# Performance work log

Measured on AMD Instinct MI355X. Metric: run time of the kernel, lower is better.

Reference implementation:

```python
import jax, jax.numpy as jnp
import numpy as np

HEADS = 8
OUT_C = 8
NEG_SLOPE = 0.2  # PyG GATConv default


def setup_inputs() -> dict:
    key = jax.random.key(0)
    k = jax.random.split(key, 6)
    N, F, E = 100000, 128, 1600000
    x = jax.random.normal(k[0], (N, F), dtype=jnp.float32)
    edge_index = jax.random.randint(k[1], (2, E), 0, N, dtype=jnp.int64)
    W = jax.random.normal(k[2], (F, HEADS * OUT_C), dtype=jnp.float32) * (1.0 / np.sqrt(F))
    att_src = jax.random.normal(k[3], (HEADS, OUT_C), dtype=jnp.float32) * 0.1
    att_dst = jax.random.normal(k[4], (HEADS, OUT_C), dtype=jnp.float32) * 0.1
    bias = jnp.zeros((HEADS * OUT_C,), dtype=jnp.float32)
    return {"x": x, "edge_index": edge_index, "W": W,
            "att_src": att_src, "att_dst": att_dst, "bias": bias}


def reference(x, edge_index, W, att_src, att_dst, bias):
    N = x.shape[0]
    # add self loops (PyG default add_self_loops=True)
    loops = jnp.arange(N, dtype=edge_index.dtype)
    src = jnp.concatenate([edge_index[0], loops])  # [E']
    dst = jnp.concatenate([edge_index[1], loops])  # [E']

    h = (x @ W).reshape(N, HEADS, OUT_C)          # [N,H,C]
    a_src = jnp.einsum('nhc,hc->nh', h, att_src)  # [N,H]
    a_dst = jnp.einsum('nhc,hc->nh', h, att_dst)  # [N,H]

    # per-edge LeakyReLU attention logits
    e = jax.nn.leaky_relu(a_src[src] + a_dst[dst], NEG_SLOPE)  # [E',H]

    # segment softmax over incoming edges of each destination node
    emax = jax.ops.segment_max(e, dst, num_segments=N)  # every node has a self loop
    ex = jnp.exp(e - emax[dst])
    denom = jax.ops.segment_sum(ex, dst, num_segments=N)
    alpha = ex / denom[dst]  # [E',H]  (dropout on alpha skipped: eval mode)

    # scatter-add weighted source features
    out = jax.ops.segment_sum(alpha[:, :, None] * h[src], dst, num_segments=N)  # [N,H,C]
    return out.reshape(N, HEADS * OUT_C) + bias
```

## Files before the change

kernel.cpp:

```cpp
#include <hip/hip_runtime.h>
#include <hip/hip_bf16.h>


#define F 128
#define HC 64
#define H 8

__device__ inline ushort f2bf(float f) {
    unsigned u = __float_as_uint(f);
    u += 0x7fff + ((u >> 16) & 1);
    return (ushort)(u >> 16);
}

__global__ __launch_bounds__(256) void k_gemm(const float* __restrict__ x,
                                              const float* __restrict__ W,
                                              const float* __restrict__ att_src,
                                              const float* __restrict__ att_dst,
                                              ushort* __restrict__ h2,
                                              float* __restrict__ a_src,
                                              float* __restrict__ a_dst, int N) {
    __shared__ float xs[64][F];
    __shared__ float Ws[F][HC];
    const int tid  = threadIdx.x;
    const int row0 = blockIdx.x * 64;
    #pragma unroll
    for (int i = 0; i < 8; ++i) {
        int idx = i * 256 + tid;
        ((float4*)Ws)[idx] = ((const float4*)W)[idx];
    }
    #pragma unroll
    for (int i = 0; i < 8; ++i) {
        int idx = i * 256 + tid;
        int r = idx >> 5;
        float4 v = make_float4(0.f, 0.f, 0.f, 0.f);
        if (row0 + r < N) v = ((const float4*)x)[(size_t)row0 * 32 + idx];
        ((float4*)xs)[idx] = v;
    }
    __syncthreads();
    const int c0 = (tid & 15) * 4;
    const int r0 = (tid >> 4) * 4;
    float acc[4][4] = {};
    for (int k = 0; k < F; k += 4) {
        float w[4][4];
        *(float4*)w[0] = *(const float4*)&Ws[k + 0][c0];
        *(float4*)w[1] = *(const float4*)&Ws[k + 1][c0];
        *(float4*)w[2] = *(const float4*)&Ws[k + 2][c0];
        *(float4*)w[3] = *(const float4*)&Ws[k + 3][c0];
        #pragma unroll
        for (int i = 0; i < 4; ++i) {
            float4 xv = *(const float4*)&xs[r0 + i][k];
            #pragma unroll
            for (int c = 0; c < 4; ++c) {
                acc[i][c] += xv.x * w[0][c];
                acc[i][c] += xv.y * w[1][c];
                acc[i][c] += xv.z * w[2][c];
                acc[i][c] += xv.w * w[3][c];
            }
        }
    }
    const int head = (tid & 15) >> 1;
    const int cb   = c0 & 7;
    float as4[4], ad4[4];
    #pragma unroll
    for (int c = 0; c < 4; ++c) {
        as4[c] = att_src[head * 8 + cb + c];
        ad4[c] = att_dst[head * 8 + cb + c];
    }
    #pragma unroll
    for (int i = 0; i < 4; ++i) {
        int r = row0 + r0 + i;
        if (r < N) {
            ushort4 pk;
            pk.x = f2bf(acc[i][0]); pk.y = f2bf(acc[i][1]);
            pk.z = f2bf(acc[i][2]); pk.w = f2bf(acc[i][3]);
            *(ushort4*)&h2[(size_t)r * HC + c0] = pk;
            float ps = acc[i][0]*as4[0] + acc[i][1]*as4[1] +
                       acc[i][2]*as4[2] + acc[i][3]*as4[3];
            float pd = acc[i][0]*ad4[0] + acc[i][1]*ad4[1] +
                       acc[i][2]*ad4[2] + acc[i][3]*ad4[3];
            ps += __shfl_xor(ps, 1);
            pd += __shfl_xor(pd, 1);
            if ((tid & 1) == 0) {
                a_src[(size_t)r * H + head] = ps;
                a_dst[(size_t)r * H + head] = pd;
            }
        }
    }
}

__global__ __launch_bounds__(1024) void k_h(const int* __restrict__ ei,
                                            int* __restrict__ hist,
                                            int E, int N, int npg) {
    extern __shared__ int lcnt[];
    const int grp = blockIdx.x & 7;
    const int lo  = grp * npg;
    const unsigned len = (unsigned)(min(N, lo + npg) - lo);
    for (int i = threadIdx.x; i < npg; i += 1024) lcnt[i] = 0;
    __syncthreads();
    const int t    = (blockIdx.x >> 3) * 1024 + threadIdx.x;
    const int nthr = (gridDim.x >> 3) * 1024;
    const int a0 = (4 - (E & 3)) & 3;
    const int nv = (E - a0) >> 2;
    const int4* vd = (const int4*)(ei + E + a0);
    for (int q = t; q < nv; q += nthr) {
        int4 d = vd[q];
        unsigned c;
        c = (unsigned)(d.x - lo); if (c < len) atomicAdd(&lcnt[c], 1);
        c = (unsigned)(d.y - lo); if (c < len) atomicAdd(&lcnt[c], 1);
        c = (unsigned)(d.z - lo); if (c < len) atomicAdd(&lcnt[c], 1);
        c = (unsigned)(d.w - lo); if (c < len) atomicAdd(&lcnt[c], 1);
    }
    if (blockIdx.x < 8) {
        int r = (E - a0) & 3;
        int e = -1;
        int tx = (int)threadIdx.x;
        if (tx < a0) e = tx;
        else if (tx - a0 < r) e = a0 + (nv << 2) + (tx - a0);
        if (e >= 0) {
            unsigned c = (unsigned)(ei[E + e] - lo);
            if (c < len) atomicAdd(&lcnt[c], 1);
        }
    }
    __syncthreads();
    int* hrow = hist + (size_t)blockIdx.x * npg;
    for (int i = threadIdx.x; i < npg; i += 1024) hrow[i] = lcnt[i];
}

__global__ __launch_bounds__(256) void k_scan1(const int* __restrict__ hist,
                                               int* __restrict__ offs,
                                               int* __restrict__ bsums,
                                               int N, int npg) {
    __shared__ int s[256];
    int i = blockIdx.x * 256 + threadIdx.x;
    int v = 0;
    if (i < N) {
        int g = i / npg;
        int c = i - g * npg;
        const int* hp = hist + (size_t)g * npg + c;
        #pragma unroll 8
        for (int j = 0; j < 32; ++j) v += hp[(size_t)(j << 3) * npg];
        v += 1;
    }
    s[threadIdx.x] = v;
    __syncthreads();
    for (int d = 1; d < 256; d <<= 1) {
        int t = (threadIdx.x >= d) ? s[threadIdx.x - d] : 0;
        __syncthreads();
        s[threadIdx.x] += t;
        __syncthreads();
    }
    if (i < N) offs[i] = s[threadIdx.x] - v;
    if (threadIdx.x == 255) bsums[blockIdx.x] = s[255];
}

__global__ __launch_bounds__(512) void k_scan2(int* __restrict__ bsums, int nb) {
    __shared__ int s[512];
    int v = (threadIdx.x < nb) ? bsums[threadIdx.x] : 0;
    s[threadIdx.x] = v;
    __syncthreads();
    for (int d = 1; d < 512; d <<= 1) {
        int t = (threadIdx.x >= d) ? s[threadIdx.x - d] : 0;
        __syncthreads();
        s[threadIdx.x] += t;
        __syncthreads();
    }
    if (threadIdx.x < nb) bsums[threadIdx.x] = s[threadIdx.x] - v;
}

__global__ __launch_bounds__(256) void k_scan3(int* __restrict__ offs,
                                               const int* __restrict__ bsums,
                                               int* __restrict__ hist,
                                               int* __restrict__ srcs,
                                               int N, int npg, int Etot) {
    int i = blockIdx.x * 256 + threadIdx.x;
    if (i == 0) offs[N] = Etot;
    if (i >= N) return;
    int o = offs[i] + bsums[blockIdx.x];
    offs[i] = o;
    srcs[o] = i;
    int p = o + 1;
    int g = i / npg;
    int c = i - g * npg;
    int* hp = hist + (size_t)g * npg + c;
    #pragma unroll 8
    for (int j = 0; j < 32; ++j) {
        int t = hp[(size_t)(j << 3) * npg];
        hp[(size_t)(j << 3) * npg] = p;
        p += t;
    }
}

__global__ __launch_bounds__(1024) void k_scat(const int* __restrict__ ei,
                                               const int* __restrict__ hist,
                                               int* __restrict__ srcs,
                                               int E, int N, int npg) {
    extern __shared__ int lpos[];
    const int grp = blockIdx.x & 7;
    const int lo  = grp * npg;
    const unsigned len = (unsigned)(min(N, lo + npg) - lo);
    const int* hrow = hist + (size_t)blockIdx.x * npg;
    for (int i = threadIdx.x; i < npg; i += 1024) lpos[i] = hrow[i];
    __syncthreads();
    const int t    = (blockIdx.x >> 3) * 1024 + threadIdx.x;
    const int nthr = (gridDim.x >> 3) * 1024;
    const int a0 = (4 - (E & 3)) & 3;
    const int nv = (E - a0) >> 2;
    const int4* vd = (const int4*)(ei + E + a0);
    for (int q = t; q < nv; q += nthr) {
        int4 d = vd[q];
        unsigned c0 = (unsigned)(d.x - lo), c1 = (unsigned)(d.y - lo),
                 c2 = (unsigned)(d.z - lo), c3 = (unsigned)(d.w - lo);
        if ((c0 < len) | (c1 < len) | (c2 < len) | (c3 < len)) {
            int e = a0 + (q << 2);
            if (c0 < len) { int p = atomicAdd(&lpos[c0], 1); srcs[p] = ei[e];     }
            if (c1 < len) { int p = atomicAdd(&lpos[c1], 1); srcs[p] = ei[e + 1]; }
            if (c2 < len) { int p = atomicAdd(&lpos[c2], 1); srcs[p] = ei[e + 2]; }
            if (c3 < len) { int p = atomicAdd(&lpos[c3], 1); srcs[p] = ei[e + 3]; }
        }
    }
    if (blockIdx.x < 8) {
        int r = (E - a0) & 3;
        int e = -1;
        int tx = (int)threadIdx.x;
        if (tx < a0) e = tx;
        else if (tx - a0 < r) e = a0 + (nv << 2) + (tx - a0);
        if (e >= 0) {
            unsigned c = (unsigned)(ei[E + e] - lo);
            if (c < len) { int p = atomicAdd(&lpos[c], 1); srcs[p] = ei[e]; }
        }
    }
}

__global__ __launch_bounds__(256) void k_gat(const int* __restrict__ offs,
                                             const int* __restrict__ srcs,
                                             const ushort* __restrict__ h2,
                                             const float* __restrict__ a_src,
                                             const float* __restrict__ a_dst,
                                             const float* __restrict__ bias,
                                             float* __restrict__ out, int N) {
    const int lane = threadIdx.x & 63;
    const int half = lane >> 5;
    const int l32  = lane & 31;
    const int g    = l32 >> 3;
    const int hd   = l32 & 7;
    const int wave = threadIdx.x >> 6;
    const int d = blockIdx.x * 8 + wave * 2 + half;
    const bool valid = d < N;

    int off = 0, end = 0;
    float adst = 0.f;
    if (valid) {
        off  = offs[d];
        end  = offs[d + 1];
        adst = a_dst[d * H + hd];
    }

    float acc[8] = {0.f, 0.f, 0.f, 0.f, 0.f, 0.f, 0.f, 0.f};
    float den = 0.f;

    for (int i = off + g; i < end; i += 4) {
        int s = srcs[i];
        float a = a_src[s * H + hd] + adst;
        a = a > 0.f ? a : 0.2f * a;
        float ex = __expf(a);
        uint4 u = *(const uint4*)(h2 + ((size_t)s << 6) + (hd << 3));
        acc[0] += ex * __uint_as_float(u.x << 16);
        acc[1] += ex * __uint_as_float(u.x & 0xffff0000u);
        acc[2] += ex * __uint_as_float(u.y << 16);
        acc[3] += ex * __uint_as_float(u.y & 0xffff0000u);
        acc[4] += ex * __uint_as_float(u.z << 16);
        acc[5] += ex * __uint_as_float(u.z & 0xffff0000u);
        acc[6] += ex * __uint_as_float(u.w << 16);
        acc[7] += ex * __uint_as_float(u.w & 0xffff0000u);
        den += ex;
    }

    #pragma unroll
    for (int m = 8; m <= 16; m <<= 1) {
        #pragma unroll
        for (int c = 0; c < 8; ++c) acc[c] += __shfl_xor(acc[c], m);
        den += __shfl_xor(den, m);
    }

    if (g == 0 && valid) {
        float r = 1.f / den;
        float4 o0, o1;
        o0.x = acc[0]*r + bias[hd*8+0]; o0.y = acc[1]*r + bias[hd*8+1];
        o0.z = acc[2]*r + bias[hd*8+2]; o0.w = acc[3]*r + bias[hd*8+3];
        o1.x = acc[4]*r + bias[hd*8+4]; o1.y = acc[5]*r + bias[hd*8+5];
        o1.z = acc[6]*r + bias[hd*8+6]; o1.w = acc[7]*r + bias[hd*8+7];
        *(float4*)&out[(size_t)d * HC + hd * 8]     = o0;
        *(float4*)&out[(size_t)d * HC + hd * 8 + 4] = o1;
    }
}

extern "C" void kernel_launch(void* const* d_in, const int* in_sizes, int n_in,
                              void* d_out, int out_size, void* d_ws, size_t ws_size,
                              hipStream_t stream) {
    const float* x       = (const float*)d_in[0];
    const int*   ei      = (const int*)d_in[1];
    const float* W       = (const float*)d_in[2];
    const float* att_src = (const float*)d_in[3];
    const float* att_dst = (const float*)d_in[4];
    const float* bias    = (const float*)d_in[5];
    const int N = in_sizes[0] / F;
    const int E = in_sizes[1] / 2;
    const int Etot = E + N;
    const int npg = (N + 7) / 8;
    float* out = (float*)d_out;

    ushort* h2    = (ushort*)d_ws;
    float*  a_src = (float*)(h2 + (size_t)N * HC);
    float*  a_dst = a_src + (size_t)N * H;
    int*    offs  = (int*)(a_dst + (size_t)N * H);
    int*    bsums = offs + N + 1;
    int*    hist  = bsums + 512;
    int*    srcs  = hist + (size_t)256 * npg;

    const int nb = (N + 255) / 256;
    const size_t ldsz = (size_t)npg * sizeof(int);
    k_gemm <<<(N + 63) / 64, 256, 0, stream>>>(x, W, att_src, att_dst, h2, a_src, a_dst, N);
    k_h    <<<256, 1024, ldsz, stream>>>(ei, hist, E, N, npg);
    k_scan1<<<nb, 256, 0, stream>>>(hist, offs, bsums, N, npg);
    k_scan2<<<1, 512, 0, stream>>>(bsums, nb);
    k_scan3<<<nb, 256, 0, stream>>>(offs, bsums, hist, srcs, N, npg, Etot);
    k_scat <<<256, 1024, ldsz, stream>>>(ei, hist, srcs, E, N, npg);
    k_gat  <<<(N + 7) / 8, 256, 0, stream>>>(offs, srcs, h2, a_src, a_dst, bias, out, N);
}
```

Measured before the change: 237.6 us.

## Double edge slices with ushort histograms, read W from global, unroll GAT loop

The CSR build now uses 512 blocks (64 slices per node group) instead of 256, and stores per-slice histograms as ushort. Scan3 writes slice-relative offsets, and the scatter kernel adds the node's CSR base from offs. The GEMM drops the shared-memory copy of W and reads it directly from global/cache. The GAT aggregation loop handles two edges per iteration to expose more memory-level parallelism. The ushort counts could overflow for very high in-degree nodes, and dropping the N bound in len relies on padding of the last group.

```diff
diff --git a/kernel.cpp b/kernel.cpp
--- a/kernel.cpp
+++ b/kernel.cpp
@@ -5,6 +5,7 @@
 #define F 128
 #define HC 64
 #define H 8
+#define NSLC 64
 
 __device__ inline ushort f2bf(float f) {
     unsigned u = __float_as_uint(f);
@@ -20,14 +21,8 @@
                                               float* __restrict__ a_src,
                                               float* __restrict__ a_dst, int N) {
     __shared__ float xs[64][F];
-    __shared__ float Ws[F][HC];
     const int tid  = threadIdx.x;
     const int row0 = blockIdx.x * 64;
-    #pragma unroll
-    for (int i = 0; i < 8; ++i) {
-        int idx = i * 256 + tid;
-        ((float4*)Ws)[idx] = ((const float4*)W)[idx];
-    }
     #pragma unroll
     for (int i = 0; i < 8; ++i) {
         int idx = i * 256 + tid;
@@ -42,10 +37,10 @@
     float acc[4][4] = {};
     for (int k = 0; k < F; k += 4) {
         float w[4][4];
-        *(float4*)w[0] = *(const float4*)&Ws[k + 0][c0];
-        *(float4*)w[1] = *(const float4*)&Ws[k + 1][c0];
-        *(float4*)w[2] = *(const float4*)&Ws[k + 2][c0];
-        *(float4*)w[3] = *(const float4*)&Ws[k + 3][c0];
+        *(float4*)w[0] = *(const float4*)&W[(size_t)(k + 0) * HC + c0];
+        *(float4*)w[1] = *(const float4*)&W[(size_t)(k + 1) * HC + c0];
+        *(float4*)w[2] = *(const float4*)&W[(size_t)(k + 2) * HC + c0];
+        *(float4*)w[3] = *(const float4*)&W[(size_t)(k + 3) * HC + c0];
         #pragma unroll
         for (int i = 0; i < 4; ++i) {
             float4 xv = *(const float4*)&xs[r0 + i][k];
@@ -89,12 +84,12 @@
 }
 
 __global__ __launch_bounds__(1024) void k_h(const int* __restrict__ ei,
-                                            int* __restrict__ hist,
-                                            int E, int N, int npg) {
+                                            ushort* __restrict__ hist,
+                                            int E, int npg) {
     extern __shared__ int lcnt[];
     const int grp = blockIdx.x & 7;
     const int lo  = grp * npg;
-    const unsigned len = (unsigned)(min(N, lo + npg) - lo);
+    const unsigned len = (unsigned)npg;
     for (int i = threadIdx.x; i < npg; i += 1024) lcnt[i] = 0;
     __syncthreads();
     const int t    = (blockIdx.x >> 3) * 1024 + threadIdx.x;
@@ -122,11 +117,11 @@
         }
     }
     __syncthreads();
-    int* hrow = hist + (size_t)blockIdx.x * npg;
-    for (int i = threadIdx.x; i < npg; i += 1024) hrow[i] = lcnt[i];
-}
-
-__global__ __launch_bounds__(256) void k_scan1(const int* __restrict__ hist,
+    ushort* hrow = hist + (size_t)blockIdx.x * npg;
+    for (int i = threadIdx.x; i < npg; i += 1024) hrow[i] = (ushort)lcnt[i];
+}
+
+__global__ __launch_bounds__(256) void k_scan1(const ushort* __restrict__ hist,
                                                int* __restrict__ offs,
                                                int* __restrict__ bsums,
                                                int N, int npg) {
@@ -136,9 +131,9 @@
     if (i < N) {
         int g = i / npg;
         int c = i - g * npg;
-        const int* hp = hist + (size_t)g * npg + c;
+        const ushort* hp = hist + (size_t)g * npg + c;
         #pragma unroll 8
-        for (int j = 0; j < 32; ++j) v += hp[(size_t)(j << 3) * npg];
+        for (int j = 0; j < NSLC; ++j) v += hp[(size_t)(j << 3) * npg];
         v += 1;
     }
     s[threadIdx.x] = v;
@@ -169,37 +164,40 @@
 
 __global__ __launch_bounds__(256) void k_scan3(int* __restrict__ offs,
                                                const int* __restrict__ bsums,
-                                               int* __restrict__ hist,
+                                               ushort* __restrict__ hist,
                                                int* __restrict__ srcs,
                                                int N, int npg, int Etot) {
     int i = blockIdx.x * 256 + threadIdx.x;
     if (i == 0) offs[N] = Etot;
     if (i >= N) return;
-    int o = offs[i] + bsums[blockIdx.x];
+    int o = offs[i] + bsums[i >> 8];
     offs[i] = o;
     srcs[o] = i;
-    int p = o + 1;
     int g = i / npg;
     int c = i - g * npg;
-    int* hp = hist + (size_t)g * npg + c;
+    ushort* hp = hist + (size_t)g * npg + c;
+    int p = 0;
     #pragma unroll 8
-    for (int j = 0; j < 32; ++j) {
-        int t = hp[(size_t)(j << 3) * npg];
-        hp[(size_t)(j << 3) * npg] = p;
+    for (int j = 0; j < NSLC; ++j) {
+        size_t off = (size_t)(j << 3) * npg;
+        int t = hp[off];
+        hp[off] = (ushort)p;
         p += t;
     }
 }
 
 __global__ __launch_bounds__(1024) void k_scat(const int* __restrict__ ei,
-                                               const int* __restrict__ hist,
+                                               const ushort* __restrict__ hist,
+                                               const int* __restrict__ offs,
                                                int* __restrict__ srcs,
-                                               int E, int N, int npg) {
+                                               int E, int npg) {
     extern __shared__ int lpos[];
     const int grp = blockIdx.x & 7;
     const int lo  = grp * npg;
-    const unsigned len = (unsigned)(min(N, lo + npg) - lo);
-    const int* hrow = hist + (size_t)blockIdx.x * npg;
-    for (int i = threadIdx.x; i < npg; i += 1024) lpos[i] = hrow[i];
+    const unsigned len = (unsigned)npg;
+    const ushort* hrow = hist + (size_t)blockIdx.x * npg;
+    for (int i = threadIdx.x; i < npg; i += 1024)
+        lpos[i] = offs[lo + i] + 1 + (int)hrow[i];
     __syncthreads();
     const int t    = (blockIdx.x >> 3) * 1024 + threadIdx.x;
     const int nthr = (gridDim.x >> 3) * 1024;
@@ -258,21 +256,36 @@
     float acc[8] = {0.f, 0.f, 0.f, 0.f, 0.f, 0.f, 0.f, 0.f};
     float den = 0.f;
 
-    for (int i = off + g; i < end; i += 4) {
-        int s = srcs[i];
-        float a = a_src[s * H + hd] + adst;
-        a = a > 0.f ? a : 0.2f * a;
-        float ex = __expf(a);
-        uint4 u = *(const uint4*)(h2 + ((size_t)s << 6) + (hd << 3));
-        acc[0] += ex * __uint_as_float(u.x << 16);
-        acc[1] += ex * __uint_as_float(u.x & 0xffff0000u);
-        acc[2] += ex * __uint_as_float(u.y << 16);
-        acc[3] += ex * __uint_as_float(u.y & 0xffff0000u);
-        acc[4] += ex * __uint_as_float(u.z << 16);
-        acc[5] += ex * __uint_as_float(u.z & 0xffff0000u);
-        acc[6] += ex * __uint_as_float(u.w << 16);
-        acc[7] += ex * __uint_as_float(u.w & 0xffff0000u);
-        den += ex;
+    for (int i = off + g; i < end; i += 8) {
+        const int i2 = i + 4;
+        const bool has1 = (i2 < end);
+        int s0 = srcs[i];
+        int s1 = has1 ? srcs[i2] : s0;
+        float a0 = a_src[s0 * H + hd] + adst;
+        float a1 = a_src[s1 * H + hd] + adst;
+        a0 = a0 > 0.f ? a0 : 0.2f * a0;
+        a1 = a1 > 0.f ? a1 : 0.2f * a1;
+        float ex0 = __expf(a0);
+        float ex1 = has1 ? __expf(a1) : 0.f;
+        uint4 u0 = *(const uint4*)(h2 + ((size_t)s0 << 6) + (hd << 3));
+        uint4 u1 = *(const uint4*)(h2 + ((size_t)s1 << 6) + (hd << 3));
+        acc[0] += ex0 * __uint_as_float(u0.x << 16);
+        acc[1] += ex0 * __uint_as_float(u0.x & 0xffff0000u);
+        acc[2] += ex0 * __uint_as_float(u0.y << 16);
+        acc[3] += ex0 * __uint_as_float(u0.y & 0xffff0000u);
+        acc[4] += ex0 * __uint_as_float(u0.z << 16);
+        acc[5] += ex0 * __uint_as_float(u0.z & 0xffff0000u);
+        acc[6] += ex0 * __uint_as_float(u0.w << 16);
+        acc[7] += ex0 * __uint_as_float(u0.w & 0xffff0000u);
+        acc[0] += ex1 * __uint_as_float(u1.x << 16);
+        acc[1] += ex1 * __uint_as_float(u1.x & 0xffff0000u);
+        acc[2] += ex1 * __uint_as_float(u1.y << 16);
+        acc[3] += ex1 * __uint_as_float(u1.y & 0xffff0000u);
+        acc[4] += ex1 * __uint_as_float(u1.z << 16);
+        acc[5] += ex1 * __uint_as_float(u1.z & 0xffff0000u);
+        acc[6] += ex1 * __uint_as_float(u1.w << 16);
+        acc[7] += ex1 * __uint_as_float(u1.w & 0xffff0000u);
+        den += ex0 + ex1;
     }
 
     #pragma unroll
@@ -314,16 +327,16 @@
     float*  a_dst = a_src + (size_t)N * H;
     int*    offs  = (int*)(a_dst + (size_t)N * H);
     int*    bsums = offs + N + 1;
-    int*    hist  = bsums + 512;
-    int*    srcs  = hist + (size_t)256 * npg;
+    ushort* hist  = (ushort*)(bsums + 512);
+    int*    srcs  = (int*)(hist + (size_t)8 * NSLC * npg);
 
     const int nb = (N + 255) / 256;
     const size_t ldsz = (size_t)npg * sizeof(int);
     k_gemm <<<(N + 63) / 64, 256, 0, stream>>>(x, W, att_src, att_dst, h2, a_src, a_dst, N);
-    k_h    <<<256, 1024, ldsz, stream>>>(ei, hist, E, N, npg);
+    k_h    <<<8 * NSLC, 1024, ldsz, stream>>>(ei, hist, E, npg);
     k_scan1<<<nb, 256, 0, stream>>>(hist, offs, bsums, N, npg);
     k_scan2<<<1, 512, 0, stream>>>(bsums, nb);
     k_scan3<<<nb, 256, 0, stream>>>(offs, bsums, hist, srcs, N, npg, Etot);
-    k_scat <<<256, 1024, ldsz, stream>>>(ei, hist, srcs, E, N, npg);
+    k_scat <<<8 * NSLC, 1024, ldsz, stream>>>(ei, hist, offs, srcs, E, npg);
     k_gat  <<<(N + 7) / 8, 256, 0, stream>>>(offs, srcs, h2, a_src, a_dst, bias, out, N);
 }
```

After: 237.8 us. Within noise of the previous version (+0.1%).
